# Performance work log

Measured on AMD Instinct MI355X. Metric: run time of the kernel, lower is better.

Reference implementation:

```python
import jax, jax.numpy as jnp
import numpy as np

T = 8388608          # sequence length (inputs reshaped to (1, T, 1) in original)
HALF_WIDTH = 0.5     # Phi hard-codes tf.constant([[1/2.0]]) regardless of width arg


def phi(v):
    # Phi(v) = v - 0.5 if v > 0.5 ; v + 0.5 if v < -0.5 ; 0 otherwise
    return jnp.where(v > HALF_WIDTH, v - HALF_WIDTH,
                     jnp.where(v < -HALF_WIDTH, v + HALF_WIDTH, jnp.zeros_like(v)))


def setup_inputs() -> dict:
    key = jax.random.key(0)
    k1, k2 = jax.random.split(key)
    x = jax.random.normal(k1, (1, T), dtype=jnp.float32)
    # learned kernel, shape (1,1), non_neg constraint -> positive init
    weight = jax.random.uniform(k2, (1, 1), dtype=jnp.float32, minval=0.5, maxval=1.5)
    state0 = jnp.zeros((1, 1), dtype=jnp.float32)
    return {"x": x, "weight": weight, "state0": state0}


def reference(x, weight, state0):
    # scale inputs by scalar kernel, flatten to the time axis: (T,)
    xs = (x * weight[0, 0]).reshape(-1)

    def step(s, xt):
        o = phi(xt - s) + s   # hysteresis update: output is also the new state
        return o, o

    s_last, outs = jax.lax.scan(step, state0[0, 0], xs)
    outputs = outs.reshape(1, T, 1)          # matches tf.keras.backend.rnn outputs_
    final_state = s_last.reshape(1, 1)       # matches states_x[-1]
    return outputs, final_state
```

## Files before the change

kernel.cpp:

```cpp
#include <hip/hip_runtime.h>
#include <math.h>


#define T_ELEMS 8388608
#define NEG_INF (-__builtin_inff())
#define POS_INF (__builtin_inff())

#define BLOCK   256
#define WAVES   4
#define F4T     8
#define F4W     (64 * F4T)
#define F4B     (BLOCK * F4T)
#define EPB     (F4B * 4)
#define NBLK    (T_ELEMS / EPB)
#define APT     (NBLK / BLOCK)

struct Op { float lo, hi; };

__device__ __forceinline__ Op combine(Op a, Op b) {
    Op r;
    r.lo = fmaxf(b.lo, fminf(b.hi, a.lo));
    r.hi = fminf(b.hi, a.hi);
    return r;
}
__device__ __forceinline__ float apply_op(Op o, float s) {
    return fmaxf(o.lo, fminf(o.hi, s));
}
__device__ __forceinline__ void fold_elem(Op& t, float e) {
    float elo = e - 0.5f, ehi = e + 0.5f;
    t.lo = fmaxf(elo, fminf(ehi, t.lo));
    t.hi = fminf(ehi, t.hi);
}
__device__ __forceinline__ void fold4(Op& t, float4 v) {
    fold_elem(t, v.x); fold_elem(t, v.y); fold_elem(t, v.z); fold_elem(t, v.w);
}
__device__ __forceinline__ int swz(int idx) { return idx ^ ((idx >> 3) & 7); }

__device__ __forceinline__ Op wave_incl_scan(Op t, int lane) {
#pragma unroll
    for (int off = 1; off < 64; off <<= 1) {
        float nlo = __shfl_up(t.lo, off);
        float nhi = __shfl_up(t.hi, off);
        if (lane >= off) {
            Op prev = { nlo, nhi };
            t = combine(prev, t);
        }
    }
    return t;
}
__device__ __forceinline__ Op wave_reduce(Op t) {
#pragma unroll
    for (int off = 1; off < 64; off <<= 1) {
        Op nb;
        nb.lo = __shfl_down(t.lo, off);
        nb.hi = __shfl_down(t.hi, off);
        t = combine(t, nb);
    }
    return t;
}

__device__ __forceinline__ void load_tile(const float4* __restrict__ xg,
                                          size_t wbase, int lane, float wv,
                                          float4* wbuf, float4 v[F4T]) {
#pragma unroll
    for (int j = 0; j < F4T; ++j) {
        float4 t = xg[wbase + j * 64 + lane];
        t.x *= wv; t.y *= wv; t.z *= wv; t.w *= wv;
        wbuf[swz(j * 64 + lane)] = t;
    }
#pragma unroll
    for (int k = 0; k < F4T; ++k)
        v[k] = wbuf[swz(lane * F4T + k)];
}

__global__ __launch_bounds__(BLOCK) void k1_agg(const float* __restrict__ x,
                                                const float* __restrict__ w,
                                                float2* __restrict__ agg) {
    __shared__ float4 xbuf[WAVES * F4W];
    __shared__ Op wt[WAVES];
    const int tid = threadIdx.x, lane = tid & 63, wid = tid >> 6;
    const int b = blockIdx.x;
    const float wv = w[0];

    float4* wbuf = xbuf + wid * F4W;
    const size_t wbase = (size_t)b * F4B + (size_t)wid * F4W;
    const float4* xg = reinterpret_cast<const float4*>(x);

    float4 v[F4T];
    load_tile(xg, wbase, lane, wv, wbuf, v);

    Op t = { v[0].x - 0.5f, v[0].x + 0.5f };
    fold_elem(t, v[0].y); fold_elem(t, v[0].z); fold_elem(t, v[0].w);
#pragma unroll
    for (int k = 1; k < F4T; ++k) fold4(t, v[k]);

    t = wave_reduce(t);
    if (lane == 0) wt[wid] = t;
    __syncthreads();
    if (tid == 0) {
        Op bt = wt[0];
#pragma unroll
        for (int k = 1; k < WAVES; ++k) bt = combine(bt, wt[k]);
        agg[b] = make_float2(bt.lo, bt.hi);
    }
}

__global__ __launch_bounds__(BLOCK) void k2_apply(const float* __restrict__ x,
                                                  const float* __restrict__ w,
                                                  const float* __restrict__ s0,
                                                  const float2* __restrict__ agg,
                                                  float* __restrict__ out) {
    __shared__ float4 xbuf[WAVES * F4W];
    __shared__ Op wtA[WAVES];
    __shared__ Op wtP[WAVES];
    const int tid = threadIdx.x, lane = tid & 63, wid = tid >> 6;
    const int b = blockIdx.x;
    const float wv = w[0];

    Op seg = { NEG_INF, POS_INF };
#pragma unroll
    for (int j = 0; j < APT; ++j) {
        int i = tid * APT + j;
        if (i < b) {
            float2 f = agg[i];
            Op o = { f.x, f.y };
            seg = combine(seg, o);
        }
    }
    seg = wave_reduce(seg);
    if (lane == 0) wtP[wid] = seg;

    float4* wbuf = xbuf + wid * F4W;
    const size_t wbase = (size_t)b * F4B + (size_t)wid * F4W;
    const float4* xg = reinterpret_cast<const float4*>(x);

    float4 v[F4T];
    load_tile(xg, wbase, lane, wv, wbuf, v);

    Op t = { v[0].x - 0.5f, v[0].x + 0.5f };
    fold_elem(t, v[0].y); fold_elem(t, v[0].z); fold_elem(t, v[0].w);
#pragma unroll
    for (int k = 1; k < F4T; ++k) fold4(t, v[k]);

    Op incl = wave_incl_scan(t, lane);
    if (lane == 63) wtA[wid] = incl;
    __syncthreads();

    Op Eb = wtP[0];
#pragma unroll
    for (int k = 1; k < WAVES; ++k) Eb = combine(Eb, wtP[k]);

    Op wpre = { NEG_INF, POS_INF };
    for (int k = 0; k < wid; ++k) wpre = combine(wpre, wtA[k]);
    float elo = __shfl_up(incl.lo, 1);
    float ehi = __shfl_up(incl.hi, 1);
    Op excl;
    if (lane == 0) { excl.lo = NEG_INF; excl.hi = POS_INF; }
    else           { excl.lo = elo;     excl.hi = ehi;     }

    float s = apply_op(Eb, s0[0]);
    s = apply_op(combine(wpre, excl), s);

    float4* og = reinterpret_cast<float4*>(out);
#pragma unroll
    for (int k = 0; k < F4T; ++k) {
        float4 e = v[k], o4;
        s = fmaxf(e.x - 0.5f, fminf(e.x + 0.5f, s)); o4.x = s;
        s = fmaxf(e.y - 0.5f, fminf(e.y + 0.5f, s)); o4.y = s;
        s = fmaxf(e.z - 0.5f, fminf(e.z + 0.5f, s)); o4.z = s;
        s = fmaxf(e.w - 0.5f, fminf(e.w + 0.5f, s)); o4.w = s;
        wbuf[swz(lane * F4T + k)] = o4;
    }
#pragma unroll
    for (int j = 0; j < F4T; ++j)
        og[wbase + j * 64 + lane] = wbuf[swz(j * 64 + lane)];

    if (b == NBLK - 1 && tid == BLOCK - 1)
        out[T_ELEMS] = s;
}

extern "C" void kernel_launch(void* const* d_in, const int* in_sizes, int n_in,
                              void* d_out, int out_size, void* d_ws, size_t ws_size,
                              hipStream_t stream) {
    const float* x  = (const float*)d_in[0];
    const float* w  = (const float*)d_in[1];
    const float* s0 = (const float*)d_in[2];
    float* out = (float*)d_out;

    float2* agg = (float2*)d_ws;

    k1_agg<<<NBLK, BLOCK, 0, stream>>>(x, w, agg);
    k2_apply<<<NBLK, BLOCK, 0, stream>>>(x, w, s0, agg, out);
}
```

Baseline: 92.34 us.

## Replace two-pass scan with single-pass decoupled look-back scan

Replaces the separate aggregate and apply kernels with one kernel using dynamic tile tickets and decoupled look-back. Each block publishes its aggregate and then its inclusive prefix through flag/value pairs, and wave 0 looks back over up to 64 predecessors at a time. This drops the second read of the input (one pass instead of two over 32MB) and a kernel launch. In exchange it adds a small init kernel, atomics and spin-waiting with inter-block serialization latency.

```diff
diff --git a/kernel.cpp b/kernel.cpp
--- a/kernel.cpp
+++ b/kernel.cpp
@@ -13,7 +13,6 @@
 #define F4B     (BLOCK * F4T)
 #define EPB     (F4B * 4)
 #define NBLK    (T_ELEMS / EPB)
-#define APT     (NBLK / BLOCK)
 
 struct Op { float lo, hi; };
 
@@ -35,6 +34,16 @@
     fold_elem(t, v.x); fold_elem(t, v.y); fold_elem(t, v.z); fold_elem(t, v.w);
 }
 __device__ __forceinline__ int swz(int idx) { return idx ^ ((idx >> 3) & 7); }
+
+__device__ __forceinline__ unsigned long long pack(Op o) {
+    float2 f = make_float2(o.lo, o.hi);
+    return __builtin_bit_cast(unsigned long long, f);
+}
+__device__ __forceinline__ Op unpack(unsigned long long p) {
+    float2 f = __builtin_bit_cast(float2, p);
+    Op o = { f.x, f.y };
+    return o;
+}
 
 __device__ __forceinline__ Op wave_incl_scan(Op t, int lane) {
 #pragma unroll
@@ -59,9 +68,39 @@
     return t;
 }
 
-__device__ __forceinline__ void load_tile(const float4* __restrict__ xg,
-                                          size_t wbase, int lane, float wv,
-                                          float4* wbuf, float4 v[F4T]) {
+__global__ void init_ws(unsigned int* ws) {
+    int i = blockIdx.x * blockDim.x + threadIdx.x;
+    if (i < 1 + 2 * NBLK) ws[i] = 0u;
+}
+
+__global__ __launch_bounds__(BLOCK) void phik(const float* __restrict__ x,
+                                              const float* __restrict__ w,
+                                              const float* __restrict__ s0,
+                                              float* __restrict__ out,
+                                              unsigned int* __restrict__ ticket,
+                                              unsigned int* __restrict__ aggFlag,
+                                              unsigned int* __restrict__ incFlag,
+                                              unsigned long long* __restrict__ aggVal,
+                                              unsigned long long* __restrict__ incVal) {
+    __shared__ float4 xbuf[WAVES * F4W];
+    __shared__ Op wtA[WAVES];
+    __shared__ Op sExcl;
+    __shared__ int sVt;
+
+    const int tid = threadIdx.x, lane = tid & 63, wid = tid >> 6;
+    const float wv = w[0];
+
+    if (tid == 0)
+        sVt = (int)__hip_atomic_fetch_add(ticket, 1u, __ATOMIC_RELAXED,
+                                          __HIP_MEMORY_SCOPE_AGENT);
+    __syncthreads();
+    const int vt = sVt;
+
+    float4* wbuf = xbuf + wid * F4W;
+    const size_t wbase = (size_t)vt * F4B + (size_t)wid * F4W;
+    const float4* xg = reinterpret_cast<const float4*>(x);
+
+    float4 v[F4T];
 #pragma unroll
     for (int j = 0; j < F4T; ++j) {
         float4 t = xg[wbase + j * 64 + lane];
@@ -71,71 +110,6 @@
 #pragma unroll
     for (int k = 0; k < F4T; ++k)
         v[k] = wbuf[swz(lane * F4T + k)];
-}
-
-__global__ __launch_bounds__(BLOCK) void k1_agg(const float* __restrict__ x,
-                                                const float* __restrict__ w,
-                                                float2* __restrict__ agg) {
-    __shared__ float4 xbuf[WAVES * F4W];
-    __shared__ Op wt[WAVES];
-    const int tid = threadIdx.x, lane = tid & 63, wid = tid >> 6;
-    const int b = blockIdx.x;
-    const float wv = w[0];
-
-    float4* wbuf = xbuf + wid * F4W;
-    const size_t wbase = (size_t)b * F4B + (size_t)wid * F4W;
-    const float4* xg = reinterpret_cast<const float4*>(x);
-
-    float4 v[F4T];
-    load_tile(xg, wbase, lane, wv, wbuf, v);
-
-    Op t = { v[0].x - 0.5f, v[0].x + 0.5f };
-    fold_elem(t, v[0].y); fold_elem(t, v[0].z); fold_elem(t, v[0].w);
-#pragma unroll
-    for (int k = 1; k < F4T; ++k) fold4(t, v[k]);
-
-    t = wave_reduce(t);
-    if (lane == 0) wt[wid] = t;
-    __syncthreads();
-    if (tid == 0) {
-        Op bt = wt[0];
-#pragma unroll
-        for (int k = 1; k < WAVES; ++k) bt = combine(bt, wt[k]);
-        agg[b] = make_float2(bt.lo, bt.hi);
-    }
-}
-
-__global__ __launch_bounds__(BLOCK) void k2_apply(const float* __restrict__ x,
-                                                  const float* __restrict__ w,
-                                                  const float* __restrict__ s0,
-                                                  const float2* __restrict__ agg,
-                                                  float* __restrict__ out) {
-    __shared__ float4 xbuf[WAVES * F4W];
-    __shared__ Op wtA[WAVES];
-    __shared__ Op wtP[WAVES];
-    const int tid = threadIdx.x, lane = tid & 63, wid = tid >> 6;
-    const int b = blockIdx.x;
-    const float wv = w[0];
-
-    Op seg = { NEG_INF, POS_INF };
-#pragma unroll
-    for (int j = 0; j < APT; ++j) {
-        int i = tid * APT + j;
-        if (i < b) {
-            float2 f = agg[i];
-            Op o = { f.x, f.y };
-            seg = combine(seg, o);
-        }
-    }
-    seg = wave_reduce(seg);
-    if (lane == 0) wtP[wid] = seg;
-
-    float4* wbuf = xbuf + wid * F4W;
-    const size_t wbase = (size_t)b * F4B + (size_t)wid * F4W;
-    const float4* xg = reinterpret_cast<const float4*>(x);
-
-    float4 v[F4T];
-    load_tile(xg, wbase, lane, wv, wbuf, v);
 
     Op t = { v[0].x - 0.5f, v[0].x + 0.5f };
     fold_elem(t, v[0].y); fold_elem(t, v[0].z); fold_elem(t, v[0].w);
@@ -146,9 +120,67 @@
     if (lane == 63) wtA[wid] = incl;
     __syncthreads();
 
-    Op Eb = wtP[0];
-#pragma unroll
-    for (int k = 1; k < WAVES; ++k) Eb = combine(Eb, wtP[k]);
+    if (wid == 0) {
+        Op blockAgg = combine(combine(combine(wtA[0], wtA[1]), wtA[2]), wtA[3]);
+        if (lane == 0) {
+            __hip_atomic_store(&aggVal[vt], pack(blockAgg), __ATOMIC_RELAXED,
+                               __HIP_MEMORY_SCOPE_AGENT);
+            __hip_atomic_store(&aggFlag[vt], 1u, __ATOMIC_RELEASE,
+                               __HIP_MEMORY_SCOPE_AGENT);
+        }
+
+        Op run = { NEG_INF, POS_INF };
+        bool done = (vt == 0);
+        int idx = vt - 1;
+        while (!done) {
+            const int wb = idx - 63;
+            const int wtile = wb + lane;
+            Op val = { NEG_INF, POS_INF };
+            int f = 0;
+            if (wtile >= 0) {
+                while (true) {
+                    if (__hip_atomic_load(&incFlag[wtile], __ATOMIC_ACQUIRE,
+                                          __HIP_MEMORY_SCOPE_AGENT)) {
+                        val = unpack(__hip_atomic_load(&incVal[wtile], __ATOMIC_RELAXED,
+                                                       __HIP_MEMORY_SCOPE_AGENT));
+                        f = 2;
+                        break;
+                    }
+                    if (__hip_atomic_load(&aggFlag[wtile], __ATOMIC_ACQUIRE,
+                                          __HIP_MEMORY_SCOPE_AGENT)) {
+                        val = unpack(__hip_atomic_load(&aggVal[wtile], __ATOMIC_RELAXED,
+                                                       __HIP_MEMORY_SCOPE_AGENT));
+                        f = 1;
+                        break;
+                    }
+                    __builtin_amdgcn_s_sleep(1);
+                }
+            }
+            const unsigned long long pmask = __ballot(f == 2);
+            if (pmask) {
+                const int p = 63 - __builtin_clzll(pmask);
+                Op contrib = (lane < p) ? Op{ NEG_INF, POS_INF } : val;
+                Op wsum = wave_reduce(contrib);
+                run = combine(wsum, run);
+                done = true;
+            } else {
+                Op wsum = wave_reduce(val);
+                run = combine(wsum, run);
+                if (wb <= 0) done = true;
+                else idx = wb - 1;
+            }
+        }
+        if (lane == 0) {
+            sExcl = run;
+            Op blockAgg2 = combine(combine(combine(wtA[0], wtA[1]), wtA[2]), wtA[3]);
+            __hip_atomic_store(&incVal[vt], pack(combine(run, blockAgg2)),
+                               __ATOMIC_RELAXED, __HIP_MEMORY_SCOPE_AGENT);
+            __hip_atomic_store(&incFlag[vt], 1u, __ATOMIC_RELEASE,
+                               __HIP_MEMORY_SCOPE_AGENT);
+        }
+    }
+    __syncthreads();
+    const Op Eb = sExcl;
 
     Op wpre = { NEG_INF, POS_INF };
     for (int k = 0; k < wid; ++k) wpre = combine(wpre, wtA[k]);
@@ -175,7 +207,7 @@
     for (int j = 0; j < F4T; ++j)
         og[wbase + j * 64 + lane] = wbuf[swz(j * 64 + lane)];
 
-    if (b == NBLK - 1 && tid == BLOCK - 1)
+    if (vt == NBLK - 1 && tid == BLOCK - 1)
         out[T_ELEMS] = s;
 }
 
@@ -187,8 +219,13 @@
     const float* s0 = (const float*)d_in[2];
     float* out = (float*)d_out;
 
-    float2* agg = (float2*)d_ws;
-
-    k1_agg<<<NBLK, BLOCK, 0, stream>>>(x, w, agg);
-    k2_apply<<<NBLK, BLOCK, 0, stream>>>(x, w, s0, agg, out);
-}
+    unsigned int* ticket  = (unsigned int*)d_ws;
+    unsigned int* aggFlag = ticket + 1;
+    unsigned int* incFlag = aggFlag + NBLK;
+    unsigned long long* aggVal = (unsigned long long*)((char*)d_ws + 16384);
+    unsigned long long* incVal = aggVal + NBLK;
+
+    init_ws<<<(1 + 2 * NBLK + 255) / 256, 256, 0, stream>>>(ticket);
+    phik<<<NBLK, BLOCK, 0, stream>>>(x, w, s0, out, ticket,
+                                     aggFlag, incFlag, aggVal, incVal);
+}
```

Measured after the change: 205.5 us. 2.23x slower.
